# Kernel tuning notes

Measured on AMD Instinct MI355X. Metric: run time of the kernel, lower is better.

The kernel has to match this reference:

```python
import jax, jax.numpy as jnp
import numpy as np

SCALE = 1.0


def _chamfer_pair(a, b):
    # a: [N,3], b: [M,3] -> (dist1 [N], dist2 [M]) squared NN distances
    # ||a-b||^2 = ||a||^2 + ||b||^2 - 2 a.b
    aa = jnp.sum(a * a, axis=-1)            # [N]
    bb = jnp.sum(b * b, axis=-1)            # [M]
    ab = jnp.einsum('nd,md->nm', a, b)      # [N,M]
    d = aa[:, None] + bb[None, :] - 2.0 * ab
    d = jnp.maximum(d, 0.0)
    return jnp.min(d, axis=1), jnp.min(d, axis=0)


def reference(p1, p2):
    # p1, p2: [B, N, 3]; scale applied before distance, matching the torch module
    a = p1 * SCALE
    b = p2 * SCALE
    dist1, dist2 = jax.vmap(_chamfer_pair)(a, b)  # [B,N], [B,M]
    # per-sample loss = mean(dist1) + mean(dist2); total averaged over batch
    per_sample = jnp.mean(dist1, axis=1) + jnp.mean(dist2, axis=1)  # [B]
    return jnp.mean(per_sample).reshape(1)


def setup_inputs() -> dict:
    key = jax.random.key(0)
    k1, k2 = jax.random.split(key)
    B, N, M = 4, 8192, 8192
    p1 = jax.random.normal(k1, (B, N, 3), dtype=jnp.float32)
    p2 = jax.random.normal(k2, (B, M, 3), dtype=jnp.float32)
    return {"p1": p1, "p2": p2}
```

## Files before the change

### kernel.cpp

```cpp
#include <hip/hip_runtime.h>
#include <math.h>

#define BATCH   4
#define NPTS    8192
#define THREADS 256
#define NQ      (2 * BATCH * NPTS)
#define TCH     16
#define CHUNK   (NPTS / TCH)
#define QPB     128
#define QTILES  (NPTS / QPB)

static constexpr float SCALE = 1.0f;

typedef __attribute__((ext_vector_type(8)))  short          bf16x8;
typedef __attribute__((ext_vector_type(8)))  unsigned short u16x8;
typedef __attribute__((ext_vector_type(16))) float          f32x16;

__device__ __forceinline__ unsigned short f2b(float f) {
    union { float f; unsigned u; } v; v.f = f;
    return (unsigned short)((v.u + 0x7FFFu + ((v.u >> 16) & 1u)) >> 16);
}
__device__ __forceinline__ float b2f(unsigned short h) {
    union { unsigned u; float f; } v; v.u = ((unsigned)h) << 16;
    return v.f;
}


__global__ __launch_bounds__(THREADS)
void chamfer_prep_kernel(const float* __restrict__ p1,
                         const float* __restrict__ p2,
                         unsigned short* __restrict__ trec,
                         unsigned short* __restrict__ qrec,
                         float* __restrict__ acc)
{
    const int id   = blockIdx.x * THREADS + threadIdx.x;
    const int role = id >> 16;
    const int slot = id & 65535;
    const int dir  = slot >> 15;
    const int rem  = slot & 32767;
    const float* tc = (dir == 0 ? p2 : p1);
    const float* qc = (dir == 0 ? p1 : p2);
    const float* src = role ? qc : tc;

    const float x = src[rem * 3 + 0] * SCALE;
    const float y = src[rem * 3 + 1] * SCALE;
    const float z = src[rem * 3 + 2] * SCALE;

    unsigned short r[16];
    const unsigned short one = 0x3F80;
    if (role == 0) {
        const unsigned short xh = f2b(x), yh = f2b(y), zh = f2b(z);
        const unsigned short xl = f2b(x - b2f(xh));
        const unsigned short yl = f2b(y - b2f(yh));
        const unsigned short zl = f2b(z - b2f(zh));
        const float bb = fmaf(z, z, fmaf(y, y, x * x));
        const unsigned short bh = f2b(bb), bl = f2b(bb - b2f(bh));
        r[0]=xh; r[1]=yh; r[2]=zh;  r[3]=xl; r[4]=yl; r[5]=zl;
        r[6]=xh; r[7]=yh; r[8]=zh;  r[9]=bh; r[10]=bl;
        r[11]=one; r[12]=one; r[13]=0; r[14]=0; r[15]=0;
        u16x8* dst = (u16x8*)(trec + (size_t)slot * 16);
        dst[0] = *(u16x8*)&r[0];
        dst[1] = *(u16x8*)&r[8];
    } else {
        const float mx = -2.0f * x, my = -2.0f * y, mz = -2.0f * z;
        const unsigned short xh = f2b(mx), yh = f2b(my), zh = f2b(mz);
        const unsigned short xl = f2b(mx - b2f(xh));
        const unsigned short yl = f2b(my - b2f(yh));
        const unsigned short zl = f2b(mz - b2f(zh));
        const float aa = fmaf(z, z, fmaf(y, y, x * x));
        const unsigned short ah = f2b(aa), al = f2b(aa - b2f(ah));
        r[0]=xh; r[1]=yh; r[2]=zh;  r[3]=xh; r[4]=yh; r[5]=zh;
        r[6]=xl; r[7]=yl; r[8]=zl;  r[9]=one; r[10]=one;
        r[11]=ah; r[12]=al; r[13]=0; r[14]=0; r[15]=0;
        u16x8* dst = (u16x8*)(qrec + (size_t)slot * 16);
        dst[0] = *(u16x8*)&r[0];
        dst[1] = *(u16x8*)&r[8];
    }
    if (id < 3) reinterpret_cast<unsigned*>(acc)[id] = 0u;
}

__global__ __launch_bounds__(THREADS, 8)
void chamfer_mfma_kernel(const unsigned short* __restrict__ trec,
                         const unsigned short* __restrict__ qrec,
                         unsigned* __restrict__ qmin_g)
{
    __shared__ unsigned short lds[CHUNK * 16];

    const int bid = blockIdx.x;
    const int c   = bid % TCH;
    const int qt  = (bid / TCH) % QTILES;
    const int b   = (bid / (TCH * QTILES)) % BATCH;
    const int dir = bid / (TCH * QTILES * BATCH);
    const int base = (dir * BATCH + b) * NPTS;

    const u16x8* tsrc = (const u16x8*)(trec + (size_t)(base + c * CHUNK) * 16);
    u16x8* l8 = (u16x8*)lds;
    #pragma unroll
    for (int i = threadIdx.x; i < CHUNK * 2; i += THREADS) l8[i] = tsrc[i];

    const int l = threadIdx.x & 63;
    const int w = threadIdx.x >> 6;
    const int qslot = base + qt * QPB + w * 32 + (l & 31);
    const bf16x8 bv = *(const bf16x8*)(qrec + ((size_t)qslot * 2 + (l >> 5)) * 8);

    __syncthreads();

    float rm = 3.0e38f;
    #pragma unroll 4
    for (int tb = 0; tb < CHUNK / 32; ++tb) {
        const bf16x8 av =
            *(const bf16x8*)&lds[(tb * 64 + (l & 31) * 2 + (l >> 5)) * 8];
        f32x16 zc = {0.f,0.f,0.f,0.f,0.f,0.f,0.f,0.f,
                     0.f,0.f,0.f,0.f,0.f,0.f,0.f,0.f};
        const f32x16 d =
            __builtin_amdgcn_mfma_f32_32x32x16_bf16(av, bv, zc, 0, 0, 0);
        const float f0 = fminf(fminf(d[0],  d[1]),  fminf(d[2],  d[3]));
        const float f1 = fminf(fminf(d[4],  d[5]),  fminf(d[6],  d[7]));
        const float f2 = fminf(fminf(d[8],  d[9]),  fminf(d[10], d[11]));
        const float f3 = fminf(fminf(d[12], d[13]), fminf(d[14], d[15]));
        rm = fminf(rm, fminf(fminf(f0, f1), fminf(f2, f3)));
    }

    rm = fminf(rm, __shfl_xor(rm, 32, 64));
    rm = fmaxf(rm, 0.0f);
    if (l < 32)
        atomicMin(&qmin_g[qslot], __float_as_uint(rm));
}

__global__ __launch_bounds__(THREADS)
void chamfer_reduce_kernel(const unsigned* __restrict__ qmin_g,
                           float* __restrict__ acc,
                           float* __restrict__ out)
{
    const int idx = blockIdx.x * THREADS + threadIdx.x;
    float m = __uint_as_float(qmin_g[idx]);

    #pragma unroll
    for (int o = 32; o > 0; o >>= 1) m += __shfl_down(m, o, 64);

    __shared__ float red[4];
    const int wave = threadIdx.x >> 6;
    const int lane = threadIdx.x & 63;
    if (lane == 0) red[wave] = m;
    __syncthreads();
    if (threadIdx.x == 0) {
        const float s = red[0] + red[1] + red[2] + red[3];
        atomicAdd(&acc[blockIdx.x >> 7], s);
        __threadfence();
        const unsigned tk = atomicAdd(reinterpret_cast<unsigned*>(acc + 2), 1u);
        if (tk == 255) {
            __threadfence();
            const float s0 = atomicAdd(&acc[0], 0.0f);
            const float s1 = atomicAdd(&acc[1], 0.0f);
            out[0] = (s0 + s1) * (1.0f / (float)(BATCH * NPTS));
        }
    }
}

extern "C" void kernel_launch(void* const* d_in, const int* in_sizes, int n_in,
                              void* d_out, int out_size, void* d_ws, size_t ws_size,
                              hipStream_t stream) {
    const float* p1 = (const float*)d_in[0];
    const float* p2 = (const float*)d_in[1];
    float* out = (float*)d_out;

    unsigned short* trec = (unsigned short*)d_ws;
    unsigned short* qrec = trec + (size_t)NQ * 16;
    unsigned*       qmin = (unsigned*)(qrec + (size_t)NQ * 16);
    float*          acc  = (float*)(qmin + NQ);

    chamfer_prep_kernel<<<2 * NQ / THREADS, THREADS, 0, stream>>>(p1, p2, trec, qrec, acc);
    chamfer_mfma_kernel<<<2 * BATCH * QTILES * TCH, THREADS, 0, stream>>>(trec, qrec, qmin);
    chamfer_reduce_kernel<<<NQ / THREADS, THREADS, 0, stream>>>(qmin, acc, out);
}
```

Measured before the change: 92.56 us.

## Process two query tiles per wave to reuse LDS target fragments

Each wave now handles 64 queries with two MFMAs per LDS-loaded target fragment, doubling queries per block and halving the number of blocks and redundant LDS staging. The target record layout is rearranged into 32-row tiles so each lane's fragment load is contiguous in LDS, avoiding the interleaved addressing and likely bank conflicts. The min-fold uses a flatter tree, and all 64 lanes now issue the atomicMin instead of half. The cost is higher register pressure from two accumulators and fewer blocks available to hide latency.

```diff
diff --git a/kernel.cpp b/kernel.cpp
--- a/kernel.cpp
+++ b/kernel.cpp
@@ -7,7 +7,8 @@
 #define NQ      (2 * BATCH * NPTS)
 #define TCH     16
 #define CHUNK   (NPTS / TCH)
-#define QPB     128
+#define TPC     (CHUNK / 32)
+#define QPB     256
 #define QTILES  (NPTS / QPB)
 
 static constexpr float SCALE = 1.0f;
@@ -58,9 +59,11 @@
         r[0]=xh; r[1]=yh; r[2]=zh;  r[3]=xl; r[4]=yl; r[5]=zl;
         r[6]=xh; r[7]=yh; r[8]=zh;  r[9]=bh; r[10]=bl;
         r[11]=one; r[12]=one; r[13]=0; r[14]=0; r[15]=0;
-        u16x8* dst = (u16x8*)(trec + (size_t)slot * 16);
-        dst[0] = *(u16x8*)&r[0];
-        dst[1] = *(u16x8*)&r[8];
+        u16x8* t8 = (u16x8*)trec;
+        const size_t tile = (size_t)(slot >> 5);
+        const int    row  = slot & 31;
+        t8[tile * 64 + row]      = *(u16x8*)&r[0];
+        t8[tile * 64 + 32 + row] = *(u16x8*)&r[8];
     } else {
         const float mx = -2.0f * x, my = -2.0f * y, mz = -2.0f * z;
         const unsigned short xh = f2b(mx), yh = f2b(my), zh = f2b(mz);
@@ -79,12 +82,22 @@
     if (id < 3) reinterpret_cast<unsigned*>(acc)[id] = 0u;
 }
 
+__device__ __forceinline__ void fold16(const f32x16 d, float& rm) {
+    const float g0 = fminf(fminf(d[0],  d[1]),  d[2]);
+    const float g1 = fminf(fminf(d[3],  d[4]),  d[5]);
+    const float g2 = fminf(fminf(d[6],  d[7]),  d[8]);
+    const float g3 = fminf(fminf(d[9],  d[10]), d[11]);
+    const float g4 = fminf(fminf(d[12], d[13]), d[14]);
+    rm = fminf(rm, fminf(fminf(fminf(g0, g1), fminf(g2, g3)),
+                         fminf(g4, d[15])));
+}
+
 __global__ __launch_bounds__(THREADS, 8)
 void chamfer_mfma_kernel(const unsigned short* __restrict__ trec,
                          const unsigned short* __restrict__ qrec,
                          unsigned* __restrict__ qmin_g)
 {
-    __shared__ unsigned short lds[CHUNK * 16];
+    __shared__ u16x8 lds8[TPC * 64];
 
     const int bid = blockIdx.x;
     const int c   = bid % TCH;
@@ -92,39 +105,42 @@
     const int b   = (bid / (TCH * QTILES)) % BATCH;
     const int dir = bid / (TCH * QTILES * BATCH);
     const int base = (dir * BATCH + b) * NPTS;
+    const int cloud_tiles = (dir * BATCH + b) * (NPTS / 32);
 
-    const u16x8* tsrc = (const u16x8*)(trec + (size_t)(base + c * CHUNK) * 16);
-    u16x8* l8 = (u16x8*)lds;
+    const u16x8* tsrc = (const u16x8*)trec
+                      + (size_t)(cloud_tiles + c * TPC) * 64;
     #pragma unroll
-    for (int i = threadIdx.x; i < CHUNK * 2; i += THREADS) l8[i] = tsrc[i];
+    for (int i = threadIdx.x; i < TPC * 64; i += THREADS) lds8[i] = tsrc[i];
 
-    const int l = threadIdx.x & 63;
-    const int w = threadIdx.x >> 6;
-    const int qslot = base + qt * QPB + w * 32 + (l & 31);
-    const bf16x8 bv = *(const bf16x8*)(qrec + ((size_t)qslot * 2 + (l >> 5)) * 8);
+    const int l  = threadIdx.x & 63;
+    const int w  = threadIdx.x >> 6;
+    const int qb = base + qt * QPB + w * 64;
+    const bf16x8 bv0 =
+        *(const bf16x8*)(qrec + ((size_t)(qb + (l & 31)) * 2 + (l >> 5)) * 8);
+    const bf16x8 bv1 =
+        *(const bf16x8*)(qrec + ((size_t)(qb + 32 + (l & 31)) * 2 + (l >> 5)) * 8);
 
     __syncthreads();
 
-    float rm = 3.0e38f;
+    float rm0 = 3.0e38f, rm1 = 3.0e38f;
+    const f32x16 zc = {0.f,0.f,0.f,0.f,0.f,0.f,0.f,0.f,
+                       0.f,0.f,0.f,0.f,0.f,0.f,0.f,0.f};
     #pragma unroll 4
-    for (int tb = 0; tb < CHUNK / 32; ++tb) {
-        const bf16x8 av =
-            *(const bf16x8*)&lds[(tb * 64 + (l & 31) * 2 + (l >> 5)) * 8];
-        f32x16 zc = {0.f,0.f,0.f,0.f,0.f,0.f,0.f,0.f,
-                     0.f,0.f,0.f,0.f,0.f,0.f,0.f,0.f};
-        const f32x16 d =
-            __builtin_amdgcn_mfma_f32_32x32x16_bf16(av, bv, zc, 0, 0, 0);
-        const float f0 = fminf(fminf(d[0],  d[1]),  fminf(d[2],  d[3]));
-        const float f1 = fminf(fminf(d[4],  d[5]),  fminf(d[6],  d[7]));
-        const float f2 = fminf(fminf(d[8],  d[9]),  fminf(d[10], d[11]));
-        const float f3 = fminf(fminf(d[12], d[13]), fminf(d[14], d[15]));
-        rm = fminf(rm, fminf(fminf(f0, f1), fminf(f2, f3)));
+    for (int tb = 0; tb < TPC; ++tb) {
+        const bf16x8 av = *(const bf16x8*)&lds8[tb * 64 + l];
+        const f32x16 d0 =
+            __builtin_amdgcn_mfma_f32_32x32x16_bf16(av, bv0, zc, 0, 0, 0);
+        fold16(d0, rm0);
+        const f32x16 d1 =
+            __builtin_amdgcn_mfma_f32_32x32x16_bf16(av, bv1, zc, 0, 0, 0);
+        fold16(d1, rm1);
     }
 
-    rm = fminf(rm, __shfl_xor(rm, 32, 64));
-    rm = fmaxf(rm, 0.0f);
-    if (l < 32)
-        atomicMin(&qmin_g[qslot], __float_as_uint(rm));
+    rm0 = fminf(rm0, __shfl_xor(rm0, 32, 64));
+    rm1 = fminf(rm1, __shfl_xor(rm1, 32, 64));
+    const float rm = fmaxf((l < 32) ? rm0 : rm1, 0.0f);
+    const int   q  = qb + (l >= 32 ? 32 : 0) + (l & 31);
+    atomicMin(&qmin_g[q], __float_as_uint(rm));
 }
 
 __global__ __launch_bounds__(THREADS)
```

Result: faster. 88.57 us (-4.3%).
